# Kernel tuning notes

Measured on AMD Instinct MI355X. Metric: run time of the kernel, lower is better.

Reference implementation:

```python
import jax, jax.numpy as jnp
import numpy as np

SCALE = 500.0  # config.scale
RADIUS = 1.1   # config.radius


def setup_inputs() -> dict:
    key = jax.random.key(0)
    k1, k2, k3 = jax.random.split(key, 3)
    N, D, T, R, B = 65536, 3, 64, 64, 64
    x = jax.random.normal(k1, (N, D), dtype=jnp.float32)
    directions = jax.random.normal(k2, (D, T), dtype=jnp.float32)
    directions = directions / jnp.linalg.norm(directions, axis=0, keepdims=True)  # unit directions
    lin = jnp.linspace(-RADIUS, RADIUS, R, dtype=jnp.float32)
    batch = jnp.sort(jax.random.randint(k3, (N,), 0, B)).astype(jnp.int64)
    return {"x": x, "directions": directions, "lin": lin, "batch": batch, "dim_size": B}


def reference(x, directions, lin, batch, dim_size):
    # nh: height of each point along each direction. [N, T]
    nh = x @ directions
    N, T = nh.shape
    R = lin.shape[0]
    # Sigmoid-smoothed indicator of (height <= threshold). [N, R, T]
    ecc = jax.nn.sigmoid(SCALE * (lin[None, :, None] - nh[:, None, :]))
    # Scatter-accumulate per point cloud. [B, R, T]
    ect = jax.ops.segment_sum(
        ecc.reshape(N, R * T), batch, num_segments=dim_size,
        indices_are_sorted=True,
    ).reshape(dim_size, R, T)
    return ect
```

## Files before the change

### kernel.cpp

```cpp
#include <hip/hip_runtime.h>


#define T_DIRS   64
#define R_STEPS  64
#define NROWS    67
#define ROWW     9
#define N_BATCH  64
#define TSPLIT   8
#define TQW      8
#define PSW      8
#define THREADS  1024
#define NWAVES   16
#define CHUNK    2048
#define SSTRIDE  64

#define RADIUS_F 1.1f
#define STEP_F   (2.0f * RADIUS_F / (R_STEPS - 1))
#define INV_STEP (1.0f / STEP_F)
#define OFF_F    (RADIUS_F * INV_STEP)
#define MEXP     (-500.0f * STEP_F * 1.4426950408889634f)
#define FIXP     16384.0f
#define FIXP_U   16384u
#define INV_FIXP (1.0f / 16384.0f)

__global__ __launch_bounds__(THREADS) void ect_kernel(
    const float* __restrict__ x,
    const float* __restrict__ dirs,
    const int*   __restrict__ batch,
    float* __restrict__ out,
    int N)
{
    __shared__ unsigned s_a[NROWS * ROWW];
    __shared__ unsigned s_ws[NWAVES * TQW];
    __shared__ float    s_x[CHUNK * 3];
    __shared__ int      s_samp[THREADS];
    __shared__ int      s_ks_lo, s_ks_hi, s_lo, s_hi;

    const int tid  = threadIdx.x;
    const int b    = blockIdx.x >> 3;
    const int q    = blockIdx.x & (TSPLIT - 1);
    const int lane = tid & 63;
    const int w    = tid >> 6;
    const int ps   = lane >> 3;
    const int tq   = lane & (TQW - 1);
    const int tg   = q * TQW + tq;

    const int nsamp = min(THREADS, (N + SSTRIDE - 1) / SSTRIDE);

    for (int i = tid; i < NROWS * ROWW; i += THREADS) s_a[i] = 0u;
    if (tid == 0) { s_ks_lo = nsamp; s_ks_hi = nsamp; s_lo = N; s_hi = N; }
    if (tid * SSTRIDE < N) s_samp[tid] = batch[tid * SSTRIDE];

    const float d0 = dirs[tg];
    const float d1 = dirs[T_DIRS + tg];
    const float d2 = dirs[2 * T_DIRS + tg];
    __syncthreads();

    if (tid < nsamp) {
        int v  = s_samp[tid];
        int vp = (tid == 0) ? -1 : s_samp[tid - 1];
        if (v >= b && vp < b)  s_ks_lo = tid;
        if (v >  b && vp <= b) s_ks_hi = tid;
    }
    __syncthreads();

    {
        int kl = s_ks_lo, kh = s_ks_hi;
        if (tid < 128) {
            int w0 = (kl == 0) ? 0 : (kl - 1) * SSTRIDE;
            int w1 = min(N, kl * SSTRIDE + 1);
            int j  = w0 + tid;
            if (j < w1) {
                int v  = batch[j];
                int vp = (j == 0) ? -1 : batch[j - 1];
                if (v >= b && vp < b) s_lo = j;
            }
        } else if (tid < 256) {
            int w0 = (kh == 0) ? 0 : (kh - 1) * SSTRIDE;
            int w1 = min(N, kh * SSTRIDE + 1);
            int j  = w0 + (tid - 128);
            if (j < w1) {
                int v  = batch[j];
                int vp = (j == 0) ? -1 : batch[j - 1];
                if (v > b && vp <= b) s_hi = j;
            }
        }
    }
    __syncthreads();
    const int lo = s_lo, hi = s_hi;

    for (int cbase = lo; cbase < hi; cbase += CHUNK) {
        const int cnt = min(CHUNK, hi - cbase);
        for (int i = tid; i < cnt * 3; i += THREADS) s_x[i] = x[cbase * 3 + i];
        __syncthreads();

        for (int p0 = 0; p0 < cnt; p0 += NWAVES * PSW) {
            int p = p0 + w * PSW + ps;
            if (p < cnt) {
                float x0 = s_x[p * 3 + 0];
                float x1 = s_x[p * 3 + 1];
                float x2 = s_x[p * 3 + 2];
                float nh  = fmaf(x2, d2, fmaf(x1, d1, x0 * d0));
                float u   = fmaf(nh, INV_STEP, OFF_F);
                float r0f = rintf(u);
                float dd  = r0f - u;
                float e   = __builtin_amdgcn_exp2f(dd * MEXP);
                float s   = __builtin_amdgcn_rcpf(1.0f + e);
                unsigned si = (unsigned)fmaf(s, FIXP, 0.5f);
                int j1 = min(max((int)r0f + 1, 0), R_STEPS + 1);
                unsigned* cell = &s_a[j1 * ROWW + tq];
                atomicAdd(cell, si);
                atomicAdd(cell + ROWW, FIXP_U - si);
            }
        }
        __syncthreads();
    }

    const int rl = ps & 3;
    unsigned v = s_a[(4 * w + 1 + rl) * ROWW + tq];
    unsigned wsum = v;
    wsum += __shfl_xor(wsum, 8, 64);
    wsum += __shfl_xor(wsum, 16, 64);
    if (ps == 0) s_ws[w * TQW + tq] = wsum;
    __syncthreads();

    if (ps < 4) {
        unsigned run = s_a[tq];
        for (int w2 = 0; w2 < w; ++w2) run += s_ws[w2 * TQW + tq];
#pragma unroll
        for (int i = 1; i <= 3; ++i)
            if (i <= rl) run += s_a[(4 * w + i) * ROWW + tq];
        run += v;
        int r = 4 * w + rl;
        out[((size_t)b << 12) | (r << 6) | tg] = (float)run * INV_FIXP;
    }
}

extern "C" void kernel_launch(void* const* d_in, const int* in_sizes, int n_in,
                              void* d_out, int out_size, void* d_ws, size_t ws_size,
                              hipStream_t stream) {
    const float* x     = (const float*)d_in[0];
    const float* dirs  = (const float*)d_in[1];
    const int*   batch = (const int*)d_in[3];
    float* out = (float*)d_out;
    const int N = in_sizes[3];

    ect_kernel<<<dim3(N_BATCH * TSPLIT), dim3(THREADS), 0, stream>>>(
        x, dirs, batch, out, N);
}
```

Before: 13.65 us.

## Split directions across more smaller blocks and read points directly from global

```diff
diff --git a/kernel.cpp b/kernel.cpp
--- a/kernel.cpp
+++ b/kernel.cpp
@@ -4,15 +4,15 @@
 #define T_DIRS   64
 #define R_STEPS  64
 #define NROWS    67
-#define ROWW     9
+#define ROWW     5
 #define N_BATCH  64
-#define TSPLIT   8
-#define TQW      8
-#define PSW      8
-#define THREADS  1024
-#define NWAVES   16
-#define CHUNK    2048
-#define SSTRIDE  64
+#define TSPLIT   16
+#define TQW      4
+#define PSW      16
+#define THREADS  512
+#define NWAVES   8
+#define SSTRIDE  256
+#define MAXSAMP  512
 
 #define RADIUS_F 1.1f
 #define STEP_F   (2.0f * RADIUS_F / (R_STEPS - 1))
@@ -32,106 +32,96 @@
 {
     __shared__ unsigned s_a[NROWS * ROWW];
     __shared__ unsigned s_ws[NWAVES * TQW];
-    __shared__ float    s_x[CHUNK * 3];
-    __shared__ int      s_samp[THREADS];
+    __shared__ int      s_samp[MAXSAMP];
     __shared__ int      s_ks_lo, s_ks_hi, s_lo, s_hi;
 
     const int tid  = threadIdx.x;
-    const int b    = blockIdx.x >> 3;
+    const int b    = blockIdx.x >> 4;
     const int q    = blockIdx.x & (TSPLIT - 1);
     const int lane = tid & 63;
     const int w    = tid >> 6;
-    const int ps   = lane >> 3;
+    const int ps   = lane >> 2;
     const int tq   = lane & (TQW - 1);
     const int tg   = q * TQW + tq;
 
-    const int nsamp = min(THREADS, (N + SSTRIDE - 1) / SSTRIDE);
+    const int nsamp = (N + SSTRIDE - 1) / SSTRIDE;
 
     for (int i = tid; i < NROWS * ROWW; i += THREADS) s_a[i] = 0u;
     if (tid == 0) { s_ks_lo = nsamp; s_ks_hi = nsamp; s_lo = N; s_hi = N; }
-    if (tid * SSTRIDE < N) s_samp[tid] = batch[tid * SSTRIDE];
+    for (int k = tid; k < nsamp; k += THREADS) s_samp[k] = batch[k * SSTRIDE];
 
     const float d0 = dirs[tg];
     const float d1 = dirs[T_DIRS + tg];
     const float d2 = dirs[2 * T_DIRS + tg];
     __syncthreads();
 
-    if (tid < nsamp) {
-        int v  = s_samp[tid];
-        int vp = (tid == 0) ? -1 : s_samp[tid - 1];
-        if (v >= b && vp < b)  s_ks_lo = tid;
-        if (v >  b && vp <= b) s_ks_hi = tid;
+    for (int k = tid; k < nsamp; k += THREADS) {
+        int v  = s_samp[k];
+        int vp = (k == 0) ? -1 : s_samp[k - 1];
+        if (v >= b && vp < b)  s_ks_lo = k;
+        if (v >  b && vp <= b) s_ks_hi = k;
     }
     __syncthreads();
 
-    {
+    if (tid <= SSTRIDE) {
         int kl = s_ks_lo, kh = s_ks_hi;
-        if (tid < 128) {
-            int w0 = (kl == 0) ? 0 : (kl - 1) * SSTRIDE;
-            int w1 = min(N, kl * SSTRIDE + 1);
-            int j  = w0 + tid;
-            if (j < w1) {
-                int v  = batch[j];
-                int vp = (j == 0) ? -1 : batch[j - 1];
-                if (v >= b && vp < b) s_lo = j;
-            }
-        } else if (tid < 256) {
-            int w0 = (kh == 0) ? 0 : (kh - 1) * SSTRIDE;
-            int w1 = min(N, kh * SSTRIDE + 1);
-            int j  = w0 + (tid - 128);
-            if (j < w1) {
-                int v  = batch[j];
-                int vp = (j == 0) ? -1 : batch[j - 1];
-                if (v > b && vp <= b) s_hi = j;
-            }
+        int w0 = (kl == 0) ? 0 : (kl - 1) * SSTRIDE;
+        int w1 = (kl >= nsamp) ? N : min(N, kl * SSTRIDE + 1);
+        int j  = w0 + tid;
+        if (j < w1) {
+            int v  = batch[j];
+            int vp = (j == 0) ? -1 : batch[j - 1];
+            if (v >= b && vp < b) s_lo = j;
+        }
+        int h0 = (kh == 0) ? 0 : (kh - 1) * SSTRIDE;
+        int h1 = (kh >= nsamp) ? N : min(N, kh * SSTRIDE + 1);
+        j = h0 + tid;
+        if (j < h1) {
+            int v  = batch[j];
+            int vp = (j == 0) ? -1 : batch[j - 1];
+            if (v > b && vp <= b) s_hi = j;
         }
     }
     __syncthreads();
     const int lo = s_lo, hi = s_hi;
+    const int len = hi - lo;
 
-    for (int cbase = lo; cbase < hi; cbase += CHUNK) {
-        const int cnt = min(CHUNK, hi - cbase);
-        for (int i = tid; i < cnt * 3; i += THREADS) s_x[i] = x[cbase * 3 + i];
-        __syncthreads();
+    for (int p = w * PSW + ps; p < len; p += NWAVES * PSW) {
+        int g = lo + p;
+        float x0 = x[g * 3 + 0];
+        float x1 = x[g * 3 + 1];
+        float x2 = x[g * 3 + 2];
+        float nh  = fmaf(x2, d2, fmaf(x1, d1, x0 * d0));
+        float u   = fmaf(nh, INV_STEP, OFF_F);
+        float r0f = rintf(u);
+        float dd  = r0f - u;
+        float e   = __builtin_amdgcn_exp2f(dd * MEXP);
+        float s   = __builtin_amdgcn_rcpf(1.0f + e);
+        unsigned si = (unsigned)fmaf(s, FIXP, 0.5f);
+        int j1 = min(max((int)r0f + 1, 0), R_STEPS + 1);
+        unsigned* cell = &s_a[j1 * ROWW + tq];
+        atomicAdd(cell, si);
+        atomicAdd(cell + ROWW, FIXP_U - si);
+    }
+    __syncthreads();
 
-        for (int p0 = 0; p0 < cnt; p0 += NWAVES * PSW) {
-            int p = p0 + w * PSW + ps;
-            if (p < cnt) {
-                float x0 = s_x[p * 3 + 0];
-                float x1 = s_x[p * 3 + 1];
-                float x2 = s_x[p * 3 + 2];
-                float nh  = fmaf(x2, d2, fmaf(x1, d1, x0 * d0));
-                float u   = fmaf(nh, INV_STEP, OFF_F);
-                float r0f = rintf(u);
-                float dd  = r0f - u;
-                float e   = __builtin_amdgcn_exp2f(dd * MEXP);
-                float s   = __builtin_amdgcn_rcpf(1.0f + e);
-                unsigned si = (unsigned)fmaf(s, FIXP, 0.5f);
-                int j1 = min(max((int)r0f + 1, 0), R_STEPS + 1);
-                unsigned* cell = &s_a[j1 * ROWW + tq];
-                atomicAdd(cell, si);
-                atomicAdd(cell + ROWW, FIXP_U - si);
-            }
-        }
-        __syncthreads();
-    }
-
-    const int rl = ps & 3;
-    unsigned v = s_a[(4 * w + 1 + rl) * ROWW + tq];
+    const int rl = ps & 7;
+    unsigned v = s_a[(8 * w + 1 + rl) * ROWW + tq];
     unsigned wsum = v;
+    wsum += __shfl_xor(wsum, 4, 64);
     wsum += __shfl_xor(wsum, 8, 64);
     wsum += __shfl_xor(wsum, 16, 64);
-    if (ps == 0) s_ws[w * TQW + tq] = wsum;
+    if (lane < TQW) s_ws[w * TQW + tq] = wsum;
     __syncthreads();
 
-    if (ps < 4) {
+    if (ps < 8) {
         unsigned run = s_a[tq];
         for (int w2 = 0; w2 < w; ++w2) run += s_ws[w2 * TQW + tq];
 #pragma unroll
-        for (int i = 1; i <= 3; ++i)
-            if (i <= rl) run += s_a[(4 * w + i) * ROWW + tq];
+        for (int i = 1; i <= 7; ++i)
+            if (i <= rl) run += s_a[(8 * w + i) * ROWW + tq];
         run += v;
-        int r = 4 * w + rl;
+        int r = 8 * w + rl;
         out[((size_t)b << 12) | (r << 6) | tg] = (float)run * INV_FIXP;
     }
 }
```

After: 12.70 us. -7.0%, faster.
